# Kernel optimization log

Hardware: AMD Instinct MI355X
Metric: run time of the kernel (lower is better)

The kernel has to match this reference:

```python
import jax, jax.numpy as jnp
import numpy as np


def conv1d(x, w, b):
    # x: [B, C_in, T], w: [C_out, C_in, K] (torch layout), b: [C_out]
    y = jax.lax.conv_general_dilated(
        x, w, window_strides=(1,), padding='SAME',
        dimension_numbers=('NCH', 'OIH', 'NCH'))
    return y + b[None, :, None]


def setup_inputs() -> dict:
    B, T, IN, H, D, K = 16, 2048, 80, 512, 512, 1024
    key = jax.random.key(0)
    ks = jax.random.split(key, 10)
    f32 = jnp.float32

    def w_init(k, shape, fan_in):
        return (jax.random.normal(k, shape, f32) / np.sqrt(fan_in)).astype(f32)

    return {
        'mels':    jax.random.normal(ks[0], (B, T, IN), f32),
        'enc_w1':  w_init(ks[1], (H, IN, 3), IN * 3),
        'enc_b1':  jnp.zeros((H,), f32),
        'enc_w2':  w_init(ks[2], (D, H, 3), H * 3),
        'enc_b2':  jnp.zeros((D,), f32),
        'codebook': jax.random.normal(ks[3], (K, D), f32),
        'dec_w1':  w_init(ks[4], (H, D, 3), D * 3),
        'dec_b1':  jnp.zeros((H,), f32),
        'dec_w2':  w_init(ks[5], (IN, H, 3), H * 3),
        'dec_b2':  jnp.zeros((IN,), f32),
    }


def reference(mels, enc_w1, enc_b1, enc_w2, enc_b2, codebook,
              dec_w1, dec_b1, dec_w2, dec_b2):
    B, T, _ = mels.shape
    D = codebook.shape[1]

    # ---- encoder: conv -> relu -> conv ----
    x = jnp.swapaxes(mels, 1, 2)                      # [B, in_dim, T]
    z = conv1d(jax.nn.relu(conv1d(x, enc_w1, enc_b1)), enc_w2, enc_b2)  # [B, D, T]

    # ---- vector quantization ----
    z_t = jnp.swapaxes(z, 1, 2)                       # [B, T, D]
    flat = z_t.reshape(-1, D)                         # [B*T, D]
    d = ((flat ** 2).sum(axis=1, keepdims=True)
         - 2.0 * flat @ codebook.T
         + (codebook ** 2).sum(axis=1)[None, :])      # [B*T, K]
    idx = jnp.argmin(d, axis=1).reshape(B, T)         # [B, T] int
    quantized = codebook[idx]                         # [B, T, D] gather

    # ---- decoder: conv -> relu -> conv ----
    q = jnp.swapaxes(quantized, 1, 2)                 # [B, D, T]
    recon = conv1d(jax.nn.relu(conv1d(q, dec_w1, dec_b1)), dec_w2, dec_b2)
    recon = jnp.swapaxes(recon, 1, 2)                 # [B, T, in_dim]
    return recon, idx
```

## Files before the change

kernel.cpp:

```cpp
#include <hip/hip_runtime.h>
#include <hip/hip_bf16.h>

#define Bsz   16
#define Tn    2048
#define INC   80
#define Hc    512
#define Dc    512
#define NCODE 1024
#define BT    (Bsz * Tn)
#define RECON_N (Bsz * Tn * INC)
#define MARGIN 0.03f

typedef __attribute__((ext_vector_type(8))) short bf16x8;
typedef __attribute__((ext_vector_type(4))) float f32x4;
typedef __attribute__((ext_vector_type(4))) unsigned short u16x4;

static __device__ __forceinline__ unsigned short f2bf(float x) {
    unsigned u = __float_as_uint(x);
    u += 0x7FFF + ((u >> 16) & 1);
    return (unsigned short)(u >> 16);
}
static __device__ __forceinline__ float bf2f(unsigned short h) {
    return __uint_as_float((unsigned)h << 16);
}

typedef const __attribute__((address_space(1))) unsigned int* gas_p;
typedef __attribute__((address_space(3))) unsigned int* las_p;
static __device__ __forceinline__ void async16(const void* g, const void* l) {
    __builtin_amdgcn_global_load_lds(
        (gas_p)(unsigned long long)g,
        (las_p)(unsigned int)(unsigned long long)l,
        16, 0, 0);
}

static __device__ __forceinline__ void wave_vm_drain() {
    asm volatile("s_waitcnt vmcnt(0)" ::: "memory");
}

__global__ __launch_bounds__(64)
void code_norms(const float* __restrict__ CB, float* __restrict__ CN) {
    int j = blockIdx.x;
    int lane = threadIdx.x;
    const float4* row = (const float4*)(CB + (size_t)j * Dc);
    float s = 0.f;
    #pragma unroll
    for (int i = 0; i < 2; ++i) {
        float4 v = row[lane + i * 64];
        s = fmaf(v.x, v.x, s);
        s = fmaf(v.y, v.y, s);
        s = fmaf(v.z, v.z, s);
        s = fmaf(v.w, v.w, s);
    }
    #pragma unroll
    for (int off = 32; off > 0; off >>= 1) s += __shfl_down(s, off, 64);
    if (lane == 0) CN[j] = s;
}

__global__ __launch_bounds__(256)
void cb_transpose(const float* __restrict__ CB, float* __restrict__ CBt) {
    const int j0 = blockIdx.x * 64;
    const int d0 = blockIdx.y * 64;
    __shared__ float ts[64][65];
    const int tid = threadIdx.x;
    for (int i = tid; i < 4096; i += 256) {
        int r = i >> 6, c = i & 63;
        ts[r][c] = CB[(size_t)(j0 + r) * Dc + d0 + c];
    }
    __syncthreads();
    for (int i = tid; i < 4096; i += 256) {
        int r = i >> 6, c = i & 63;
        CBt[(size_t)(d0 + r) * NCODE + j0 + c] = ts[c][r];
    }
}

__global__ __launch_bounds__(256)
void mels_transpose(const float* __restrict__ M, float* __restrict__ MT) {
    const int t0 = blockIdx.x * 64;
    const int b  = blockIdx.y;
    __shared__ float ts[64][84];
    const int tid = threadIdx.x;
    #pragma unroll
    for (int it = 0; it < 5; ++it) {
        int i = tid + it * 256;
        int t = i / 20, c4 = i % 20;
        *(float4*)&ts[t][c4 * 4] =
            *(const float4*)&M[((size_t)b * Tn + t0 + t) * INC + c4 * 4];
    }
    __syncthreads();
    #pragma unroll
    for (int it = 0; it < 20; ++it) {
        int i = tid + it * 256;
        int c = i >> 6, t = i & 63;
        MT[((size_t)b * INC + c) * Tn + t0 + t] = ts[t][c];
    }
}

__global__ __launch_bounds__(256)
void wt_transpose(const float* __restrict__ W, float* __restrict__ Wt,
                  int Cin, int Cout) {
    const int o0 = blockIdx.x * 64;
    const int c0 = blockIdx.y * 16;
    __shared__ float ts[48][65];
    const int tid = threadIdx.x;
    for (int i = tid; i < 64 * 48; i += 256) {
        int o = i / 48, ck = i % 48;
        int oo = o0 + o;
        float v = 0.f;
        if (oo < Cout) v = W[(size_t)oo * Cin * 3 + c0 * 3 + ck];
        ts[ck][o] = v;
    }
    __syncthreads();
    for (int i = tid; i < 48 * 64; i += 256) {
        int o = i & 63, ck = i >> 6;
        int oo = o0 + o;
        if (oo < Cout) Wt[(size_t)(c0 * 3 + ck) * Cout + oo] = ts[ck][o];
    }
}

__global__ __launch_bounds__(256)
void wsplit(const float* __restrict__ W, unsigned short* __restrict__ Whl) {
    int o = blockIdx.x, k = blockIdx.y;
    #pragma unroll
    for (int it = 0; it < 2; ++it) {
        int c = threadIdx.x + it * 256;
        float v = W[((size_t)o * Hc + c) * 3 + k];
        unsigned short h = f2bf(v);
        size_t base = ((size_t)(k * Hc + o) * 16 + (c >> 5)) * 64 + (c & 31);
        Whl[base] = h;
        Whl[base + 32] = f2bf(v - bf2f(h));
    }
}

__global__ __launch_bounds__(256)
void wsplit80(const float* __restrict__ W, unsigned short* __restrict__ Wh) {
    int o = blockIdx.x, k = blockIdx.y;
    #pragma unroll
    for (int it = 0; it < 2; ++it) {
        int c = threadIdx.x + it * 256;
        Wh[((size_t)k * INC + o) * Hc + c] = f2bf(W[((size_t)o * Hc + c) * 3 + k]);
    }
}

__global__ __launch_bounds__(256)
void cbsplit(const float* __restrict__ CB, unsigned short* __restrict__ CBhl) {
    int j = blockIdx.x;
    #pragma unroll
    for (int it = 0; it < 2; ++it) {
        int d = threadIdx.x + it * 256;
        float v = CB[(size_t)j * Dc + d];
        unsigned short h = f2bf(v);
        size_t base = ((size_t)j * 16 + (d >> 5)) * 64 + (d & 31);
        CBhl[base] = h;
        CBhl[base + 32] = f2bf(v - bf2f(h));
    }
}

__global__ __launch_bounds__(256)
void conv_enc1(const float* __restrict__ X, const float* __restrict__ Wt,
               const float* __restrict__ bias, unsigned short* __restrict__ Yhl) {
    const int t0 = blockIdx.x * 64;
    const int o0 = blockIdx.y * 128;
    const int b  = blockIdx.z;
    union SharedU {
        struct { float Xs[16][72]; float Ws[48][132]; } a;
        float Ys[128][69];
    };
    __shared__ __align__(16) SharedU su;
    float (&Xs)[16][72]  = su.a.Xs;
    float (&Ws)[48][132] = su.a.Ws;
    const int tid = threadIdx.x;
    const int tx = tid & 15, ty = tid >> 4;
    float acc[8][4] = {};
    const float* Xb = X + (size_t)b * INC * Tn;

    if (blockIdx.x == 0 && tid < 64) {
        u16x4 z4 = {0, 0, 0, 0};
        *(u16x4*)(Yhl + ((size_t)(b * (Tn + 2)) * 16 + (o0 >> 5)) * 64 + tid * 4) = z4;
    }
    if (blockIdx.x == Tn / 64 - 1 && tid < 64) {
        u16x4 z4 = {0, 0, 0, 0};
        *(u16x4*)(Yhl + ((size_t)(b * (Tn + 2) + Tn + 1) * 16 + (o0 >> 5)) * 64
                  + tid * 4) = z4;
    }

    for (int c0 = 0; c0 < INC; c0 += 16) {
        for (int i = tid; i < 16 * 66; i += 256) {
            int cc = i / 66, tt = i % 66;
            int t = t0 + tt - 1;
            float v = 0.f;
            if (t >= 0 && t < Tn) v = Xb[(size_t)(c0 + cc) * Tn + t];
            Xs[cc][tt] = v;
        }
        for (int i = tid; i < 48 * 128; i += 256) {
            int o = i & 127, ck = i >> 7;
            Ws[ck][o] = Wt[(size_t)(c0 * 3 + ck) * Hc + o0 + o];
        }
        __syncthreads();
        #pragma unroll
        for (int cc = 0; cc < 16; ++cc) {
            float4 xa = *(const float4*)&Xs[cc][tx * 4];
            float2 xb2 = *(const float2*)&Xs[cc][tx * 4 + 4];
            float xv[6] = {xa.x, xa.y, xa.z, xa.w, xb2.x, xb2.y};
            #pragma unroll
            for (int k = 0; k < 3; ++k) {
                float4 wa = *(const float4*)&Ws[cc * 3 + k][ty * 4];
                float4 wb = *(const float4*)&Ws[cc * 3 + k][64 + ty * 4];
                float wv[8] = {wa.x, wa.y, wa.z, wa.w, wb.x, wb.y, wb.z, wb.w};
                #pragma unroll
                for (int i8 = 0; i8 < 8; ++i8)
                    #pragma unroll
                    for (int j = 0; j < 4; ++j)
                        acc[i8][j] = fmaf(wv[i8], xv[k + j], acc[i8][j]);
            }
        }
        __syncthreads();
    }
    #pragma unroll
    for (int og = 0; og < 2; ++og)
        #pragma unroll
        for (int oi = 0; oi < 4; ++oi) {
            int ol = og * 64 + ty * 4 + oi;
            float bv = bias[o0 + ol];
            const int i8 = og * 4 + oi;
            #pragma unroll
            for (int j = 0; j < 4; ++j)
                su.Ys[ol][tx * 4 + j] = fmaxf(acc[i8][j] + bv, 0.f);
        }
    __syncthreads();
    #pragma unroll
    for (int it = 0; it < 8; ++it) {
        int i = tid + it * 256;
        int oq = i & 31, t = i >> 5;
        int o4 = o0 + oq * 4;
        u16x4 h, l;
        #pragma unroll
        for (int r = 0; r < 4; ++r) {
            float v = su.Ys[oq * 4 + r][t];
            unsigned short hh = f2bf(v);
            h[r] = hh;
            l[r] = f2bf(v - bf2f(hh));
        }
        size_t base = ((size_t)(b * (Tn + 2) + 1 + t0 + t) * 16 + (o4 >> 5)) * 64
                      + (o4 & 31);
        *(u16x4*)(Yhl + base) = h;
        *(u16x4*)(Yhl + base + 32) = l;
    }
}

__global__ __launch_bounds__(256)
void conv_mid_mfma(const unsigned short* __restrict__ Xhl,
                   const unsigned short* __restrict__ Whl,
                   const float* __restrict__ bias,
                   unsigned short* __restrict__ Zt,
                   unsigned short* __restrict__ Lo2) {
    const int lin  = blockIdx.x + (blockIdx.y << 4) + (blockIdx.z << 6);
    const int slot = lin >> 3;
    const int b  = ((lin & 7) << 1) | (slot >> 6);
    const int t0 = ((slot & 63) >> 2) << 7;
    const int o0 = (slot & 3) << 7;
    __shared__ __align__(16) unsigned short pool[4 * 2 * 72 * 64];
    const int tid  = threadIdx.x;
    const int lane = tid & 63;
    const int wave = tid >> 6;
    const int wm = wave >> 1, wn = wave & 1;
    const int m16 = lane & 15;
    const int q = lane >> 4;
    const int lrow = lane >> 3;
    const int lchk = (lane & 7) ^ lrow;
    unsigned short* XW = pool + wave * (2 * 72 * 64);
    const unsigned short* XbW = Xhl + ((size_t)b * (Tn + 2) + t0 + wn * 64) * 1024
                                + (size_t)lrow * 1024 + lchk * 8;

    f32x4 acc[4][4];
    #pragma unroll
    for (int mt = 0; mt < 4; ++mt)
        #pragma unroll
        for (int nt = 0; nt < 4; ++nt)
            acc[mt][nt] = (f32x4){0.f, 0.f, 0.f, 0.f};

    #pragma unroll
    for (int i = 0; i < 9; ++i)
        async16(XbW + (size_t)i * 8192, XW + i * 512);

    for (int c0 = 0; c0 < Hc; c0 += 32) {
        const int buf = (c0 >> 5) & 1;
        wave_vm_drain();
        if (c0 + 32 < Hc) {
            const unsigned short* src = XbW + (size_t)((c0 >> 5) + 1) * 64;
            #pragma unroll
            for (int i = 0; i < 9; ++i)
                async16(src + (size_t)i * 8192, XW + (buf ^ 1) * 4608 + i * 512);
        }
        #pragma unroll
        for (int k = 0; k < 3; ++k) {
            bf16x8 Ah[4], Al[4];
            #pragma unroll
            for (int mt = 0; mt < 4; ++mt) {
                int o = o0 + wm * 64 + mt * 16 + m16;
                size_t base = ((size_t)(k * Hc + o) * 16 + (c0 >> 5)) * 64 + q * 8;
                Ah[mt] = *(const bf16x8*)(Whl + base);
                Al[mt] = *(const bf16x8*)(Whl + base + 32);
            }
            #pragma unroll
            for (int nt = 0; nt < 4; ++nt) {
                int row = nt * 16 + m16 + k;
                const unsigned short* rp = XW + buf * 4608 + row * 64;
                int ph = (q ^ (row & 7)) * 8;
                union { bf16x8 v; uint4 u; } bh, bl;
                bh.u = *(const uint4*)(rp + ph);
                bl.u = *(const uint4*)(rp + (ph ^ 32));
                __builtin_amdgcn_s_setprio(1);
                #pragma unroll
                for (int mt = 0; mt < 4; ++mt)
                    acc[mt][nt] = __builtin_amdgcn_mfma_f32_16x16x32_bf16(
                        Ah[mt], bh.v, acc[mt][nt], 0, 0, 0);
                #pragma unroll
                for (int mt = 0; mt < 4; ++mt)
                    acc[mt][nt] = __builtin_amdgcn_mfma_f32_16x16x32_bf16(
                        Al[mt], bh.v, acc[mt][nt], 0, 0, 0);
                #pragma unroll
                for (int mt = 0; mt < 4; ++mt)
                    acc[mt][nt] = __builtin_amdgcn_mfma_f32_16x16x32_bf16(
                        Ah[mt], bl.v, acc[mt][nt], 0, 0, 0);
                __builtin_amdgcn_s_setprio(0);
            }
        }
    }
    __syncthreads();
    unsigned short* SZ = pool;
    unsigned short* SL = pool + 32 * 264;
    unsigned short* Lb = Lo2 + (size_t)b * Tn * 512;
    const int g0 = o0 >> 5;
    #pragma unroll
    for (int p = 0; p < 4; ++p) {
        if (p) __syncthreads();
        if (wn == (p >> 1)) {
            #pragma unroll
            for (int nt2 = 0; nt2 < 2; ++nt2) {
                int nt = (p & 1) * 2 + nt2;
                int srow = nt2 * 16 + m16;
                #pragma unroll
                for (int mt = 0; mt < 4; ++mt) {
                    int lo = wm * 64 + mt * 16 + q * 4;
                    int ob = o0 + lo;
                    float4 bq = *(const float4*)&bias[ob];
                    float bqa[4] = {bq.x, bq.y, bq.z, bq.w};
                    u16x4 h, l, l2;
                    #pragma unroll
                    for (int r = 0; r < 4; ++r) {
                        float v = acc[mt][nt][r] + bqa[r];
                        unsigned short hh = f2bf(v);
                        float r1 = v - bf2f(hh);
                        unsigned short ll = f2bf(r1);
                        h[r] = hh;
                        l[r] = ll;
                        l2[r] = f2bf(r1 - bf2f(ll));
                    }
                    int gb = (lo >> 5) * 64 + (lo & 31);
                    *(u16x4*)&SZ[srow * 264 + gb] = h;
                    *(u16x4*)&SZ[srow * 264 + gb + 32] = l;
                    *(u16x4*)&SL[srow * 136 + lo] = l2;
                }
            }
        }
        __syncthreads();
        #pragma unroll
        for (int it = 0; it < 8; ++it) {
            int i = tid + it * 256;
            int row = i >> 6, c = i & 63;
            *(u16x4*)(Zt + ((size_t)(b * Tn + t0 + p * 32 + row) * 16 + g0) * 64
                      + c * 4) = *(u16x4*)&SZ[row * 264 + c * 4];
        }
        #pragma unroll
        for (int it = 0; it < 4; ++it) {
            int i = tid + it * 256;
            int row = i >> 5, c = i & 31;
            *(u16x4*)(Lb + (size_t)(t0 + p * 32 + row) * 512 + o0 + c * 4)
                = *(u16x4*)&SL[row * 136 + c * 4];
        }
    }
}

__global__ __launch_bounds__(256)
void dec2_mfma(const unsigned short* __restrict__ Xt,
               const unsigned short* __restrict__ Wh2,
               const float* __restrict__ bias, float* __restrict__ OUT) {
    const int t0 = blockIdx.x * 128;
    const int b  = blockIdx.z;
    __shared__ __align__(16) unsigned short XL[2][136 * 64];
    const int tid = threadIdx.x;
    const int lane = tid & 63;
    const int wave = tid >> 6;
    const int wn = wave;
    const int m16 = lane & 15;
    const int q = lane >> 4;
    const int lrow = lane >> 3;
    const int lchk = (lane & 7) ^ lrow;
    const unsigned short* Xb = Xt + ((size_t)b * (Tn + 2) + t0) * 512
                               + (size_t)lrow * 512 + lchk * 8;

    f32x4 acc[5][2];
    #pragma unroll
    for (int mt = 0; mt < 5; ++mt)
        #pragma unroll
        for (int nt = 0; nt < 2; ++nt)
            acc[mt][nt] = (f32x4){0.f, 0.f, 0.f, 0.f};

    #pragma unroll
    for (int i = 0; i < 5; ++i) {
        int ii = wave + i * 4;
        if (ii < 17)
            async16(Xb + (size_t)ii * 4096, &XL[0][ii * 512]);
    }

    for (int c0 = 0; c0 < Hc; c0 += 64) {
        const int buf = (c0 >> 6) & 1;
        __syncthreads();
        if (c0 + 64 < Hc) {
            const unsigned short* src = Xb + (size_t)((c0 >> 6) + 1) * 64;
            #pragma unroll
            for (int i = 0; i < 5; ++i) {
                int ii = wave + i * 4;
                if (ii < 17)
                    async16(src + (size_t)ii * 4096, &XL[buf ^ 1][ii * 512]);
            }
        }
        #pragma unroll
        for (int k = 0; k < 3; ++k) {
            #pragma unroll
            for (int sub = 0; sub < 2; ++sub) {
                int c = c0 + sub * 32;
                bf16x8 Ah[5];
                #pragma unroll
                for (int mt = 0; mt < 5; ++mt) {
                    int o = mt * 16 + m16;
                    Ah[mt] = *(const bf16x8*)(Wh2 + ((size_t)(k * INC + o)) * Hc
                                              + c + q * 8);
                }
                #pragma unroll
                for (int nt = 0; nt < 2; ++nt) {
                    int row = wn * 32 + nt * 16 + m16 + k;
                    const unsigned short* rp = &XL[buf][row * 64];
                    int p = sub * 4 + q;
                    int ph = (p ^ (row & 7)) * 8;
                    union { bf16x8 v; uint4 u; } bh;
                    bh.u = *(const uint4*)(rp + ph);
                    #pragma unroll
                    for (int mt = 0; mt < 5; ++mt)
                        acc[mt][nt] = __builtin_amdgcn_mfma_f32_16x16x32_bf16(
                            Ah[mt], bh.v, acc[mt][nt], 0, 0, 0);
                }
            }
        }
    }
    #pragma unroll
    for (int mt = 0; mt < 5; ++mt) {
        float4 bq = *(const float4*)&bias[mt * 16 + q * 4];
        #pragma unroll
        for (int nt = 0; nt < 2; ++nt) {
            int t = t0 + wn * 32 + nt * 16 + m16;
            float4 r;
            r.x = acc[mt][nt][0] + bq.x;
            r.y = acc[mt][nt][1] + bq.y;
            r.z = acc[mt][nt][2] + bq.z;
            r.w = acc[mt][nt][3] + bq.w;
            *(float4*)(OUT + ((size_t)b * Tn + t) * INC + mt * 16 + q * 4) = r;
        }
    }
}

__global__ __launch_bounds__(256)
void vq_mfma(const unsigned short* __restrict__ Zt,
             const unsigned short* __restrict__ CBhl,
             const float* __restrict__ CN,
             float* __restrict__ candv, int* __restrict__ candi,
             float* __restrict__ cand2v) {
    const int lin  = blockIdx.x + (blockIdx.y << 8);
    const int slotB = lin >> 3;
    const int nb = ((lin & 7) << 5) | (slotB & 31);
    const int jb = slotB >> 5;
    const int b  = nb >> 4;
    const int t0 = (nb & 15) * 128;
    const int jbase = jb * 128;
    __shared__ __align__(16) unsigned short vpool[4 * 2 * 64 * 64];
    float* RV = (float*)vpool;
    int*   RI = (int*)((char*)vpool + 4096);
    float* R2 = (float*)((char*)vpool + 8192);

    const int tid = threadIdx.x;
    const int lane = tid & 63;
    const int wave = tid >> 6;
    const int wm = wave >> 1, wn = wave & 1;
    const int m16 = lane & 15;
    const int q = lane >> 4;
    const int lrow = lane >> 3;
    const int lchk = (lane & 7) ^ lrow;
    unsigned short* XW = vpool + wave * (2 * 64 * 64);
    const unsigned short* ZbW = Zt + (size_t)(b * Tn + t0 + wn * 64) * 1024
                                + (size_t)lrow * 1024 + lchk * 8;

    f32x4 acc[4][4];
    #pragma unroll
    for (int mt = 0; mt < 4; ++mt)
        #pragma unroll
        for (int nt = 0; nt < 4; ++nt)
            acc[mt][nt] = (f32x4){0.f, 0.f, 0.f, 0.f};

    #pragma unroll
    for (int i = 0; i < 8; ++i)
        async16(ZbW + (size_t)i * 8192, XW + i * 512);

    for (int d0 = 0; d0 < Dc; d0 += 32) {
        const int buf = (d0 >> 5) & 1;
        wave_vm_drain();
        if (d0 + 32 < Dc) {
            const unsigned short* src = ZbW + (size_t)((d0 >> 5) + 1) * 64;
            #pragma unroll
            for (int i = 0; i < 8; ++i)
                async16(src + (size_t)i * 8192, XW + (buf ^ 1) * 4096 + i * 512);
        }
        bf16x8 Ah[4], Al[4];
        #pragma unroll
        for (int mt = 0; mt < 4; ++mt) {
            int j = jbase + wm * 64 + mt * 16 + m16;
            size_t base = ((size_t)j * 16 + (d0 >> 5)) * 64 + q * 8;
            Ah[mt] = *(const bf16x8*)(CBhl + base);
            Al[mt] = *(const bf16x8*)(CBhl + base + 32);
        }
        #pragma unroll
        for (int nt = 0; nt < 4; ++nt) {
            int row = nt * 16 + m16;
            const unsigned short* rp = XW + buf * 4096 + row * 64;
            int ph = (q ^ (row & 7)) * 8;
            union { bf16x8 v; uint4 u; } bh, bl;
            bh.u = *(const uint4*)(rp + ph);
            bl.u = *(const uint4*)(rp + (ph ^ 32));
            __builtin_amdgcn_s_setprio(1);
            #pragma unroll
            for (int mt = 0; mt < 4; ++mt)
                acc[mt][nt] = __builtin_amdgcn_mfma_f32_16x16x32_bf16(
                    Ah[mt], bh.v, acc[mt][nt], 0, 0, 0);
            #pragma unroll
            for (int mt = 0; mt < 4; ++mt)
                acc[mt][nt] = __builtin_amdgcn_mfma_f32_16x16x32_bf16(
                    Al[mt], bh.v, acc[mt][nt], 0, 0, 0);
            #pragma unroll
            for (int mt = 0; mt < 4; ++mt)
                acc[mt][nt] = __builtin_amdgcn_mfma_f32_16x16x32_bf16(
                    Ah[mt], bl.v, acc[mt][nt], 0, 0, 0);
            __builtin_amdgcn_s_setprio(0);
        }
    }
    __syncthreads();

    float cn4[4][4];
    #pragma unroll
    for (int mt = 0; mt < 4; ++mt) {
        float4 c = *(const float4*)&CN[jbase + wm * 64 + mt * 16 + q * 4];
        cn4[mt][0] = c.x; cn4[mt][1] = c.y; cn4[mt][2] = c.z; cn4[mt][3] = c.w;
    }
    #pragma unroll
    for (int nt = 0; nt < 4; ++nt) {
        int t = wn * 64 + nt * 16 + m16;
        float v1 = 1e30f, v2 = 1e30f;
        int i1 = 0;
        #pragma unroll
        for (int mt = 0; mt < 4; ++mt)
            #pragma unroll
            for (int r = 0; r < 4; ++r) {
                float d = fmaf(-2.f, acc[mt][nt][r], cn4[mt][r]);
                int j = jbase + wm * 64 + mt * 16 + q * 4 + r;
                if (d < v1 || (d == v1 && j < i1)) { v2 = v1; v1 = d; i1 = j; }
                else if (d < v2) v2 = d;
            }
        int slotw = wm * 4 + q;
        RV[t * 8 + slotw] = v1;
        RI[t * 8 + slotw] = i1;
        R2[t * 8 + slotw] = v2;
    }
    __syncthreads();
    if (tid < 128) {
        int t = tid;
        float v1 = RV[t * 8], v2 = R2[t * 8];
        int i1 = RI[t * 8];
        #pragma unroll
        for (int s = 1; s < 8; ++s) {
            float a1 = RV[t * 8 + s], a2 = R2[t * 8 + s];
            int ai = RI[t * 8 + s];
            if (a1 < v1 || (a1 == v1 && ai < i1)) {
                v2 = fminf(v1, a2); v1 = a1; i1 = ai;
            } else {
                v2 = fminf(v2, a1);
            }
        }
        int n = b * Tn + t0 + t;
        candv[(size_t)jb * BT + n] = v1;
        candi[(size_t)jb * BT + n] = i1;
        cand2v[(size_t)jb * BT + n] = v2;
    }
}

__global__ __launch_bounds__(256)
void vq_reduce2(const float* __restrict__ candv, const int* __restrict__ candi,
                const float* __restrict__ cand2v, int* __restrict__ idxI,
                float* __restrict__ idxf, int* __restrict__ flagn,
                int* __restrict__ flaglist) {
    int n = blockIdx.x * 256 + threadIdx.x;
    float v1 = candv[n], v2 = cand2v[n];
    int i1 = candi[n];
    #pragma unroll
    for (int jq = 1; jq < 8; ++jq) {
        float a1 = candv[(size_t)jq * BT + n];
        float a2 = cand2v[(size_t)jq * BT + n];
        int ai = candi[(size_t)jq * BT + n];
        if (a1 < v1 || (a1 == v1 && ai < i1)) {
            v2 = fminf(v1, a2); v1 = a1; i1 = ai;
        } else {
            v2 = fminf(v2, a1);
        }
    }
    idxI[n] = i1;
    idxf[n] = (float)i1;
    if (v2 - v1 < MARGIN) {
        int s = atomicAdd(flagn, 1);
        flaglist[s] = n;
    }
}

__global__ __launch_bounds__(256)
void vq_rescue(const int* __restrict__ flagn, const int* __restrict__ flaglist,
               const unsigned short* __restrict__ Zt,
               const unsigned short* __restrict__ Lo2,
               const float* __restrict__ CB,
               const float* __restrict__ CN, int* __restrict__ idxI,
               float* __restrict__ idxf) {
    __shared__ float zs[512];
    __shared__ float rvv[256];
    __shared__ int   rii[256];
    const int nf = *flagn;
    for (int f = blockIdx.x; f < nf; f += gridDim.x) {
        int n = flaglist[f];
        __syncthreads();
        #pragma unroll
        for (int it = 0; it < 2; ++it) {
            int d = threadIdx.x + it * 256;
            const unsigned short* zr = Zt + ((size_t)n * 16 + (d >> 5)) * 64
                                       + (d & 31);
            zs[d] = bf2f(zr[0]) + bf2f(zr[32]) + bf2f(Lo2[(size_t)n * 512 + d]);
        }
        __syncthreads();
        float bv = 1e30f;
        int bi = 0;
        #pragma unroll
        for (int jj = 0; jj < 4; ++jj) {
            int j = threadIdx.x * 4 + jj;
            const float* cr = CB + (size_t)j * Dc;
            float dot = 0.f;
            for (int d = 0; d < Dc; ++d) dot = fmaf(zs[d], cr[d], dot);
            float dist = fmaf(-2.f, dot, CN[j]);
            if (dist < bv || (dist == bv && j < bi)) { bv = dist; bi = j; }
        }
        rvv[threadIdx.x] = bv;
        rii[threadIdx.x] = bi;
        __syncthreads();
        for (int off = 128; off > 0; off >>= 1) {
            if (threadIdx.x < off) {
                float ov = rvv[threadIdx.x + off];
                int oi = rii[threadIdx.x + off];
                if (ov < rvv[threadIdx.x] ||
                    (ov == rvv[threadIdx.x] && oi < rii[threadIdx.x])) {
                    rvv[threadIdx.x] = ov; rii[threadIdx.x] = oi;
                }
            }
            __syncthreads();
        }
        if (threadIdx.x == 0) {
            idxI[n] = rii[0];
            idxf[n] = (float)rii[0];
        }
    }
}

__global__ __launch_bounds__(256)
void gemm_g(const float* __restrict__ CBt, const float* __restrict__ Wt,
            float* __restrict__ G) {
    const int j0 = blockIdx.x * 64;
    const int kk = blockIdx.y >> 2;
    const int o0 = (blockIdx.y & 3) * 128;
    __shared__ __align__(16) float As[16][68];
    __shared__ __align__(16) float Bs[16][132];
    const int tid = threadIdx.x;
    const int tx = tid & 15, ty = tid >> 4;
    float acc[4][8] = {};

    for (int c0 = 0; c0 < Dc; c0 += 16) {
        {
            int cc = tid >> 4, j4 = tid & 15;
            *(float4*)&As[cc][j4 * 4] =
                *(const float4*)&CBt[(size_t)(c0 + cc) * NCODE + j0 + j4 * 4];
        }
        #pragma unroll
        for (int it = 0; it < 2; ++it) {
            int i = tid + it * 256;
            int cc = i >> 5, o4 = i & 31;
            *(float4*)&Bs[cc][o4 * 4] =
                *(const float4*)&Wt[(size_t)((c0 + cc) * 3 + kk) * Hc + o0 + o4 * 4];
        }
        __syncthreads();
        #pragma unroll
        for (int cc = 0; cc < 16; ++cc) {
            float4 a = *(const float4*)&As[cc][tx * 4];
            float av[4] = {a.x, a.y, a.z, a.w};
            float4 b0 = *(const float4*)&Bs[cc][ty * 4];
            float4 b1 = *(const float4*)&Bs[cc][64 + ty * 4];
            float bv[8] = {b0.x, b0.y, b0.z, b0.w, b1.x, b1.y, b1.z, b1.w};
            #pragma unroll
            for (int jj = 0; jj < 4; ++jj)
                #pragma unroll
                for (int oo = 0; oo < 8; ++oo)
                    acc[jj][oo] = fmaf(av[jj], bv[oo], acc[jj][oo]);
        }
        __syncthreads();
    }
    #pragma unroll
    for (int jj = 0; jj < 4; ++jj) {
        int j = j0 + tx * 4 + jj;
        float* gp = G + (size_t)j * 1536 + kk * 512 + o0;
        *(float4*)(gp + ty * 4) = *(float4*)&acc[jj][0];
        *(float4*)(gp + 64 + ty * 4) = *(float4*)&acc[jj][4];
    }
}

__global__ __launch_bounds__(256)
void dec_y3(const int* __restrict__ idx, const float* __restrict__ G,
            const float* __restrict__ bias, unsigned short* __restrict__ Yt) {
    const int t0 = blockIdx.x * 64;
    const int o0 = blockIdx.y * 128;
    const int b  = blockIdx.z;
    const int tid = threadIdx.x;
    __shared__ int sidx[66];
    __shared__ __align__(16) float Ys[128][68];

    if (blockIdx.x == 0 && tid < 32) {
        u16x4 z4 = {0, 0, 0, 0};
        *(u16x4*)(Yt + (size_t)(b * (Tn + 2)) * 512 + o0 + tid * 4) = z4;
    }
    if (blockIdx.x == Tn / 64 - 1 && tid < 32) {
        u16x4 z4 = {0, 0, 0, 0};
        *(u16x4*)(Yt + (size_t)(b * (Tn + 2) + Tn + 1) * 512 + o0 + tid * 4) = z4;
    }

    if (tid < 66) {
        int t = t0 + tid - 1;
        sidx[tid] = (t >= 0 && t < Tn) ? idx[b * Tn + t] : -1;
    }
    __syncthreads();

    const int o = tid & 127;
    const int half = tid >> 7;
    float acc[32] = {};
    #pragma unroll
    for (int kk = 0; kk < 3; ++kk) {
        const float* Gk = G + (size_t)kk * 512 + o0 + o;
        #pragma unroll
        for (int k = 0; k < 32; ++k) {
            int j = sidx[half + 2 * k + kk];
            if (j >= 0) acc[k] += Gk[(size_t)j * 1536];
        }
    }
    float bv = bias[o0 + o];
    #pragma unroll
    for (int k = 0; k < 32; ++k)
        Ys[o][half + 2 * k] = fmaxf(acc[k] + bv, 0.f);
    __syncthreads();

    unsigned short* Yb = Yt + ((size_t)(b * (Tn + 2) + 1 + t0)) * 512 + o0;
    #pragma unroll
    for (int it = 0; it < 8; ++it) {
        int i = tid + it * 256;
        int t = i >> 5, oq = i & 31;
        u16x4 h;
        #pragma unroll
        for (int r = 0; r < 4; ++r)
            h[r] = f2bf(Ys[oq * 4 + r][t]);
        *(u16x4*)(Yb + (size_t)t * 512 + oq * 4) = h;
    }
}

extern "C" void kernel_launch(void* const* d_in, const int* in_sizes, int n_in,
                              void* d_out, int out_size, void* d_ws, size_t ws_size,
                              hipStream_t stream) {
    const float* mels    = (const float*)d_in[0];
    const float* enc_w1  = (const float*)d_in[1];
    const float* enc_b1  = (const float*)d_in[2];
    const float* enc_w2  = (const float*)d_in[3];
    const float* enc_b2  = (const float*)d_in[4];
    const float* codebook= (const float*)d_in[5];
    const float* dec_w1  = (const float*)d_in[6];
    const float* dec_b1  = (const float*)d_in[7];
    const float* dec_w2  = (const float*)d_in[8];
    const float* dec_b2  = (const float*)d_in[9];

    float* out = (float*)d_out;
    float* recon = out;
    float* idxf  = out + RECON_N;

    const size_t ACT = (size_t)Bsz * Hc * Tn;
    const size_t Y1HL_U = (size_t)Bsz * (Tn + 2) * 1024 + 16384;
    const size_t R2F = Y1HL_U / 2;

    unsigned short* Zt  = (unsigned short*)d_ws;
    unsigned short* y3t = (unsigned short*)d_ws;
    float* r2 = (float*)d_ws + ACT;
    unsigned short* y1hl = (unsigned short*)r2;
    float* sm    = r2 + R2F;
    int*   idxI  = (int*)sm;
    float* cn    = (float*)(idxI + BT);
    float* cbt   = cn + NCODE;
    float* wt1   = cbt + (size_t)Dc * NCODE;
    float* wt3   = wt1 + (size_t)INC * 3 * Hc;
    float* candv = wt3 + (size_t)Dc * 3 * Hc;
    float* cand2v= candv + (size_t)8 * BT;
    int*   candi = (int*)(cand2v + (size_t)8 * BT);
    int*   flagn = candi + (size_t)8 * BT;
    int*   flaglist = flagn + 4;
    float* G     = (float*)(flaglist + BT);
    unsigned short* whl  = (unsigned short*)(G + (size_t)NCODE * 1536);
    unsigned short* cbhl = whl + (size_t)3 * Hc * 1024;
    unsigned short* wh2  = cbhl + (size_t)NCODE * 1024;
    float* melsT = (float*)(wh2 + (size_t)3 * INC * Hc);
    unsigned short* lo2 = (unsigned short*)melsT;

    dim3 blk(256);
    hipMemsetAsync(flagn, 0, 16, stream);
    code_norms<<<dim3(NCODE), dim3(64), 0, stream>>>(codebook, cn);
    cb_transpose<<<dim3(NCODE / 64, Dc / 64), blk, 0, stream>>>(codebook, cbt);
    mels_transpose<<<dim3(Tn / 64, Bsz), blk, 0, stream>>>(mels, melsT);
    wt_transpose<<<dim3(Hc / 64, INC / 16), blk, 0, stream>>>(enc_w1, wt1, INC, Hc);
    wsplit<<<dim3(Hc, 3), blk, 0, stream>>>(enc_w2, whl);
    cbsplit<<<dim3(NCODE), blk, 0, stream>>>(codebook, cbhl);
    wt_transpose<<<dim3(Hc / 64, Dc / 16), blk, 0, stream>>>(dec_w1, wt3, Dc, Hc);
    wsplit80<<<dim3(INC, 3), blk, 0, stream>>>(dec_w2, wh2);
    gemm_g<<<dim3(NCODE / 64, 12), blk, 0, stream>>>(cbt, wt3, G);
    conv_enc1<<<dim3(Tn / 64, Hc / 128, Bsz), blk, 0, stream>>>(melsT, wt1, enc_b1,
                                                                y1hl);
    conv_mid_mfma<<<dim3(Tn / 128, Hc / 128, Bsz), blk, 0, stream>>>(y1hl, whl,
                                                                     enc_b2,
                                                                     Zt, lo2);
    vq_mfma<<<dim3(BT / 128, NCODE / 128), blk, 0, stream>>>(Zt, cbhl, cn,
                                                             candv, candi, cand2v);
    vq_reduce2<<<dim3(BT / 256), blk, 0, stream>>>(candv, candi, cand2v, idxI,
                                                   idxf, flagn, flaglist);
    vq_rescue<<<dim3(128), blk, 0, stream>>>(flagn, flaglist, Zt, lo2, codebook,
                                             cn, idxI, idxf);
    dec_y3<<<dim3(Tn / 64, 4, Bsz), blk, 0, stream>>>(idxI, G, dec_b1, y3t);
    dec2_mfma<<<dim3(Tn / 128, 1, Bsz), blk, 0, stream>>>(y3t, wh2, dec_b2, recon);
}
```

Before: 800.0 us.

## Prepack MFMA A-fragments and software-pipeline weight loads in conv and VQ kernels

Weights and codebook are split into bf16 hi/lo and stored in a fragment-major layout, so each lane reads a contiguous 16-byte chunk per MFMA tile. Inside conv_mid_mfma and vq_mfma, the A fragments for the next k-tap or d-chunk are loaded into a second register set while the current one feeds the MFMAs, which hides global load latency behind compute. The VQ loop is unrolled by two with a fixed double-buffer. The s_setprio hints are dropped. Holding extra fragment sets raises register pressure and may lower occupancy.

```diff
diff --git a/kernel.cpp b/kernel.cpp
--- a/kernel.cpp
+++ b/kernel.cpp
@@ -35,6 +35,18 @@
 
 static __device__ __forceinline__ void wave_vm_drain() {
     asm volatile("s_waitcnt vmcnt(0)" ::: "memory");
+}
+
+struct AFrag { bf16x8 h[4]; bf16x8 l[4]; };
+
+static __device__ __forceinline__ void load_afrag(
+        const unsigned short* __restrict__ Wf, int blk0, int lane, AFrag& A) {
+    #pragma unroll
+    for (int mt = 0; mt < 4; ++mt) {
+        const unsigned short* p = Wf + ((size_t)(blk0 + mt) << 10) + lane * 8;
+        A.h[mt] = *(const bf16x8*)p;
+        A.l[mt] = *(const bf16x8*)(p + 512);
+    }
 }
 
 __global__ __launch_bounds__(64)
@@ -118,16 +130,20 @@
 }
 
 __global__ __launch_bounds__(256)
-void wsplit(const float* __restrict__ W, unsigned short* __restrict__ Whl) {
+void wsplit(const float* __restrict__ W, unsigned short* __restrict__ Wf) {
     int o = blockIdx.x, k = blockIdx.y;
+    int og = o >> 4;
     #pragma unroll
     for (int it = 0; it < 2; ++it) {
         int c = threadIdx.x + it * 256;
         float v = W[((size_t)o * Hc + c) * 3 + k];
         unsigned short h = f2bf(v);
-        size_t base = ((size_t)(k * Hc + o) * 16 + (c >> 5)) * 64 + (c & 31);
-        Whl[base] = h;
-        Whl[base + 32] = f2bf(v - bf2f(h));
+        int cg = c >> 5;
+        int l = (o & 15) | (((c >> 3) & 3) << 4);
+        int e = c & 7;
+        size_t base = ((size_t)((k * 16 + cg) * 32 + og) << 10) + l * 8 + e;
+        Wf[base] = h;
+        Wf[base + 512] = f2bf(v - bf2f(h));
     }
 }
 
@@ -142,16 +158,20 @@
 }
 
 __global__ __launch_bounds__(256)
-void cbsplit(const float* __restrict__ CB, unsigned short* __restrict__ CBhl) {
+void cbsplit(const float* __restrict__ CB, unsigned short* __restrict__ CBf) {
     int j = blockIdx.x;
+    int jg = j >> 4;
     #pragma unroll
     for (int it = 0; it < 2; ++it) {
         int d = threadIdx.x + it * 256;
         float v = CB[(size_t)j * Dc + d];
         unsigned short h = f2bf(v);
-        size_t base = ((size_t)j * 16 + (d >> 5)) * 64 + (d & 31);
-        CBhl[base] = h;
-        CBhl[base + 32] = f2bf(v - bf2f(h));
+        int dg = d >> 5;
+        int l = (j & 15) | (((d >> 3) & 3) << 4);
+        int e = d & 7;
+        size_t base = ((size_t)(dg * 64 + jg) << 10) + l * 8 + e;
+        CBf[base] = h;
+        CBf[base + 512] = f2bf(v - bf2f(h));
     }
 }
 
@@ -249,7 +269,7 @@
 
 __global__ __launch_bounds__(256)
 void conv_mid_mfma(const unsigned short* __restrict__ Xhl,
-                   const unsigned short* __restrict__ Whl,
+                   const unsigned short* __restrict__ Wf,
                    const float* __restrict__ bias,
                    unsigned short* __restrict__ Zt,
                    unsigned short* __restrict__ Lo2) {
@@ -267,6 +287,7 @@
     const int q = lane >> 4;
     const int lrow = lane >> 3;
     const int lchk = (lane & 7) ^ lrow;
+    const int ogb = (o0 >> 4) + wm * 4;
     unsigned short* XW = pool + wave * (2 * 72 * 64);
     const unsigned short* XbW = Xhl + ((size_t)b * (Tn + 2) + t0 + wn * 64) * 1024
                                 + (size_t)lrow * 1024 + lchk * 8;
@@ -281,51 +302,53 @@
     #pragma unroll
     for (int i = 0; i < 9; ++i)
         async16(XbW + (size_t)i * 8192, XW + i * 512);
+    AFrag A0, A1, A2;
+    load_afrag(Wf, (0 * 16 + 0) * 32 + ogb, lane, A0);
+
+#define COMPUTE_K(KK, AF)                                                   \
+    {                                                                       \
+        _Pragma("unroll")                                                   \
+        for (int nt = 0; nt < 4; ++nt) {                                    \
+            int row = nt * 16 + m16 + (KK);                                 \
+            const unsigned short* rp = XW + buf * 4608 + row * 64;          \
+            int ph = (q ^ (row & 7)) * 8;                                   \
+            union { bf16x8 v; uint4 u; } bh, bl;                            \
+            bh.u = *(const uint4*)(rp + ph);                                \
+            bl.u = *(const uint4*)(rp + (ph ^ 32));                         \
+            _Pragma("unroll")                                               \
+            for (int mt = 0; mt < 4; ++mt)                                  \
+                acc[mt][nt] = __builtin_amdgcn_mfma_f32_16x16x32_bf16(      \
+                    (AF).h[mt], bh.v, acc[mt][nt], 0, 0, 0);                \
+            _Pragma("unroll")                                               \
+            for (int mt = 0; mt < 4; ++mt)                                  \
+                acc[mt][nt] = __builtin_amdgcn_mfma_f32_16x16x32_bf16(      \
+                    (AF).l[mt], bh.v, acc[mt][nt], 0, 0, 0);                \
+            _Pragma("unroll")                                               \
+            for (int mt = 0; mt < 4; ++mt)                                  \
+                acc[mt][nt] = __builtin_amdgcn_mfma_f32_16x16x32_bf16(      \
+                    (AF).h[mt], bl.v, acc[mt][nt], 0, 0, 0);                \
+        }                                                                   \
+    }
 
     for (int c0 = 0; c0 < Hc; c0 += 32) {
-        const int buf = (c0 >> 5) & 1;
+        const int cg = c0 >> 5;
+        const int buf = cg & 1;
         wave_vm_drain();
         if (c0 + 32 < Hc) {
-            const unsigned short* src = XbW + (size_t)((c0 >> 5) + 1) * 64;
+            const unsigned short* src = XbW + (size_t)(cg + 1) * 64;
             #pragma unroll
             for (int i = 0; i < 9; ++i)
                 async16(src + (size_t)i * 8192, XW + (buf ^ 1) * 4608 + i * 512);
         }
-        #pragma unroll
-        for (int k = 0; k < 3; ++k) {
-            bf16x8 Ah[4], Al[4];
-            #pragma unroll
-            for (int mt = 0; mt < 4; ++mt) {
-                int o = o0 + wm * 64 + mt * 16 + m16;
-                size_t base = ((size_t)(k * Hc + o) * 16 + (c0 >> 5)) * 64 + q * 8;
-                Ah[mt] = *(const bf16x8*)(Whl + base);
-                Al[mt] = *(const bf16x8*)(Whl + base + 32);
-            }
-            #pragma unroll
-            for (int nt = 0; nt < 4; ++nt) {
-                int row = nt * 16 + m16 + k;
-                const unsigned short* rp = XW + buf * 4608 + row * 64;
-                int ph = (q ^ (row & 7)) * 8;
-                union { bf16x8 v; uint4 u; } bh, bl;
-                bh.u = *(const uint4*)(rp + ph);
-                bl.u = *(const uint4*)(rp + (ph ^ 32));
-                __builtin_amdgcn_s_setprio(1);
-                #pragma unroll
-                for (int mt = 0; mt < 4; ++mt)
-                    acc[mt][nt] = __builtin_amdgcn_mfma_f32_16x16x32_bf16(
-                        Ah[mt], bh.v, acc[mt][nt], 0, 0, 0);
-                #pragma unroll
-                for (int mt = 0; mt < 4; ++mt)
-                    acc[mt][nt] = __builtin_amdgcn_mfma_f32_16x16x32_bf16(
-                        Al[mt], bh.v, acc[mt][nt], 0, 0, 0);
-                #pragma unroll
-                for (int mt = 0; mt < 4; ++mt)
-                    acc[mt][nt] = __builtin_amdgcn_mfma_f32_16x16x32_bf16(
-                        Ah[mt], bl.v, acc[mt][nt], 0, 0, 0);
-                __builtin_amdgcn_s_setprio(0);
-            }
-        }
-    }
+        load_afrag(Wf, (1 * 16 + cg) * 32 + ogb, lane, A1);
+        COMPUTE_K(0, A0);
+        load_afrag(Wf, (2 * 16 + cg) * 32 + ogb, lane, A2);
+        COMPUTE_K(1, A1);
+        load_afrag(Wf, (0 * 16 + cg + 1) * 32 + ogb, lane, A0);
+        COMPUTE_K(2, A2);
+    }
+#undef COMPUTE_K
+
     __syncthreads();
     unsigned short* SZ = pool;
     unsigned short* SL = pool + 32 * 264;
@@ -471,7 +494,7 @@
 
 __global__ __launch_bounds__(256)
 void vq_mfma(const unsigned short* __restrict__ Zt,
-             const unsigned short* __restrict__ CBhl,
+             const unsigned short* __restrict__ CBf,
              const float* __restrict__ CN,
              float* __restrict__ candv, int* __restrict__ candi,
              float* __restrict__ cand2v) {
@@ -495,6 +518,7 @@
     const int q = lane >> 4;
     const int lrow = lane >> 3;
     const int lchk = (lane & 7) ^ lrow;
+    const int jgb = jb * 8 + wm * 4;
     unsigned short* XW = vpool + wave * (2 * 64 * 64);
     const unsigned short* ZbW = Zt + (size_t)(b * Tn + t0 + wn * 64) * 1024
                                 + (size_t)lrow * 1024 + lchk * 8;
@@ -509,48 +533,55 @@
     #pragma unroll
     for (int i = 0; i < 8; ++i)
         async16(ZbW + (size_t)i * 8192, XW + i * 512);
-
-    for (int d0 = 0; d0 < Dc; d0 += 32) {
-        const int buf = (d0 >> 5) & 1;
+    AFrag Aa, Ab;
+    load_afrag(CBf, 0 * 64 + jgb, lane, Aa);
+
+#define VQ_COMPUTE(AF, BUF)                                                 \
+    {                                                                       \
+        _Pragma("unroll")                                                   \
+        for (int nt = 0; nt < 4; ++nt) {                                    \
+            int row = nt * 16 + m16;                                        \
+            const unsigned short* rp = XW + (BUF) * 4096 + row * 64;        \
+            int ph = (q ^ (row & 7)) * 8;                                   \
+            union { bf16x8 v; uint4 u; } bh, bl;                            \
+            bh.u = *(const uint4*)(rp + ph);                                \
+            bl.u = *(const uint4*)(rp + (ph ^ 32));                         \
+            _Pragma("unroll")                                               \
+            for (int mt = 0; mt < 4; ++mt)                                  \
+                acc[mt][nt] = __builtin_amdgcn_mfma_f32_16x16x32_bf16(      \
+                    (AF).h[mt], bh.v, acc[mt][nt], 0, 0, 0);                \
+            _Pragma("unroll")                                               \
+            for (int mt = 0; mt < 4; ++mt)                                  \
+                acc[mt][nt] = __builtin_amdgcn_mfma_f32_16x16x32_bf16(      \
+                    (AF).l[mt], bh.v, acc[mt][nt], 0, 0, 0);                \
+            _Pragma("unroll")                                               \
+            for (int mt = 0; mt < 4; ++mt)                                  \
+                acc[mt][nt] = __builtin_amdgcn_mfma_f32_16x16x32_bf16(      \
+                    (AF).h[mt], bl.v, acc[mt][nt], 0, 0, 0);                \
+        }                                                                   \
+    }
+
+    for (int it = 0; it < 16; it += 2) {
         wave_vm_drain();
-        if (d0 + 32 < Dc) {
-            const unsigned short* src = ZbW + (size_t)((d0 >> 5) + 1) * 64;
+        {
+            const unsigned short* src = ZbW + (size_t)(it + 1) * 64;
             #pragma unroll
             for (int i = 0; i < 8; ++i)
-                async16(src + (size_t)i * 8192, XW + (buf ^ 1) * 4096 + i * 512);
-        }
-        bf16x8 Ah[4], Al[4];
-        #pragma unroll
-        for (int mt = 0; mt < 4; ++mt) {
-            int j = jbase + wm * 64 + mt * 16 + m16;
-            size_t base = ((size_t)j * 16 + (d0 >> 5)) * 64 + q * 8;
-            Ah[mt] = *(const bf16x8*)(CBhl + base);
-            Al[mt] = *(const bf16x8*)(CBhl + base + 32);
-        }
-        #pragma unroll
-        for (int nt = 0; nt < 4; ++nt) {
-            int row = nt * 16 + m16;
-            const unsigned short* rp = XW + buf * 4096 + row * 64;
-            int ph = (q ^ (row & 7)) * 8;
-            union { bf16x8 v; uint4 u; } bh, bl;
-            bh.u = *(const uint4*)(rp + ph);
-            bl.u = *(const uint4*)(rp + (ph ^ 32));
-            __builtin_amdgcn_s_setprio(1);
-            #pragma unroll
-            for (int mt = 0; mt < 4; ++mt)
-                acc[mt][nt] = __builtin_amdgcn_mfma_f32_16x16x32_bf16(
-                    Ah[mt], bh.v, acc[mt][nt], 0, 0, 0);
-            #pragma unroll
-            for (int mt = 0; mt < 4; ++mt)
-                acc[mt][nt] = __builtin_amdgcn_mfma_f32_16x16x32_bf16(
-                    Al[mt], bh.v, acc[mt][nt], 0, 0, 0);
-            #pragma unroll
-            for (int mt = 0; mt < 4; ++mt)
-                acc[mt][nt] = __builtin_amdgcn_mfma_f32_16x16x32_bf16(
-                    Ah[mt], bl.v, acc[mt][nt], 0, 0, 0);
-            __builtin_amdgcn_s_setprio(0);
-        }
-    }
+                async16(src + (size_t)i * 8192, XW + 4096 + i * 512);
+        }
+        load_afrag(CBf, (it + 1) * 64 + jgb, lane, Ab);
+        VQ_COMPUTE(Aa, 0);
+        wave_vm_drain();
+        if (it + 2 < 16) {
+            const unsigned short* src = ZbW + (size_t)(it + 2) * 64;
+            #pragma unroll
+            for (int i = 0; i < 8; ++i)
+                async16(src + (size_t)i * 8192, XW + i * 512);
+            load_afrag(CBf, (it + 2) * 64 + jgb, lane, Aa);
+        }
+        VQ_COMPUTE(Ab, 1);
+    }
+#undef VQ_COMPUTE
     __syncthreads();
 
     float cn4[4][4];
@@ -825,9 +856,9 @@
     int*   flagn = candi + (size_t)8 * BT;
     int*   flaglist = flagn + 4;
     float* G     = (float*)(flaglist + BT);
-    unsigned short* whl  = (unsigned short*)(G + (size_t)NCODE * 1536);
-    unsigned short* cbhl = whl + (size_t)3 * Hc * 1024;
-    unsigned short* wh2  = cbhl + (size_t)NCODE * 1024;
+    unsigned short* wf  = (unsigned short*)(G + (size_t)NCODE * 1536);
+    unsigned short* cbf = wf + (size_t)3 * Hc * 1024;
+    unsigned short* wh2 = cbf + (size_t)NCODE * 1024;
     float* melsT = (float*)(wh2 + (size_t)3 * INC * Hc);
     unsigned short* lo2 = (unsigned short*)melsT;
 
@@ -837,17 +868,17 @@
     cb_transpose<<<dim3(NCODE / 64, Dc / 64), blk, 0, stream>>>(codebook, cbt);
     mels_transpose<<<dim3(Tn / 64, Bsz), blk, 0, stream>>>(mels, melsT);
     wt_transpose<<<dim3(Hc / 64, INC / 16), blk, 0, stream>>>(enc_w1, wt1, INC, Hc);
-    wsplit<<<dim3(Hc, 3), blk, 0, stream>>>(enc_w2, whl);
-    cbsplit<<<dim3(NCODE), blk, 0, stream>>>(codebook, cbhl);
+    wsplit<<<dim3(Hc, 3), blk, 0, stream>>>(enc_w2, wf);
+    cbsplit<<<dim3(NCODE), blk, 0, stream>>>(codebook, cbf);
     wt_transpose<<<dim3(Hc / 64, Dc / 16), blk, 0, stream>>>(dec_w1, wt3, Dc, Hc);
     wsplit80<<<dim3(INC, 3), blk, 0, stream>>>(dec_w2, wh2);
     gemm_g<<<dim3(NCODE / 64, 12), blk, 0, stream>>>(cbt, wt3, G);
     conv_enc1<<<dim3(Tn / 64, Hc / 128, Bsz), blk, 0, stream>>>(melsT, wt1, enc_b1,
                                                                 y1hl);
-    conv_mid_mfma<<<dim3(Tn / 128, Hc / 128, Bsz), blk, 0, stream>>>(y1hl, whl,
+    conv_mid_mfma<<<dim3(Tn / 128, Hc / 128, Bsz), blk, 0, stream>>>(y1hl, wf,
                                                                      enc_b2,
                                                                      Zt, lo2);
-    vq_mfma<<<dim3(BT / 128, NCODE / 128), blk, 0, stream>>>(Zt, cbhl, cn,
+    vq_mfma<<<dim3(BT / 128, NCODE / 128), blk, 0, stream>>>(Zt, cbf, cn,
                                                              candv, candi, cand2v);
     vq_reduce2<<<dim3(BT / 256), blk, 0, stream>>>(candv, candi, cand2v, idxI,
                                                    idxf, flagn, flaglist);
```

New measurement: 665.9 us (median of 2 runs). -16.8%, faster.
